# Kernel optimization log

Hardware: AMD Instinct MI355X
Metric: run time of the kernel (lower is better)

The kernel has to match this reference:

```python
import jax, jax.numpy as jnp
import numpy as np
from functools import partial

TAU = 2.0          # leak
VTH = 1.0          # threshold_value
DECAY = 1.0 - 1.0 / TAU  # decay_input=False, v_reset=0: v = v*(1-1/tau) + x
PAD = 3
STRIDE = 1


def heaviside(x):
    # forward of spikingjelly surrogate.ATan (surrogate only changes backward)
    return (x >= 0).astype(x.dtype)


def lif(v, inp):
    """One LIF step: charge, fire, hard reset (v_reset=0)."""
    v = v * DECAY + inp
    s = heaviside(v - VTH)
    v = v * (1.0 - s)
    return v, s


def setup_inputs() -> dict:
    key = jax.random.key(0)
    k1, k2, k3, k4 = jax.random.split(key, 4)
    B, L = 64, 2048
    C, H, NC, K = 128, 256, 10, 7
    x = jax.random.normal(k1, (B, L), dtype=jnp.float32)
    conv_w = jax.random.normal(k2, (C, 1, K), dtype=jnp.float32) * (1.0 / np.sqrt(K))
    W1 = jax.random.normal(k3, (H, C), dtype=jnp.float32) * (1.0 / np.sqrt(C))
    W2 = jax.random.normal(k4, (NC, H), dtype=jnp.float32) * (1.0 / np.sqrt(H))
    return {"x": x, "conv_w": conv_w, "W1": W1, "W2": W2}


def _forward(x, conv_w, W1, W2):
    B = x.shape[0]
    C, H, NC = conv_w.shape[0], W1.shape[0], W2.shape[0]
    # Conv1d(1 -> C): [B, 1, L] -> [B, C, T]
    xc = jax.lax.conv_general_dilated(
        x[:, None, :], conv_w, window_strides=(STRIDE,),
        padding=[(PAD, PAD)], dimension_numbers=("NCH", "OIH", "NCH"))
    T = xc.shape[2]
    xt = jnp.transpose(xc, (2, 0, 1))  # [T, B, C]

    def step(carry, x_t):
        v1, v2, v3, acc = carry
        v1, s1 = lif(v1, x_t)                       # conv LIF  [B, C]
        v2, s2 = lif(v2, s1 @ W1.T)                 # hidden LIF [B, H]
        v3, s3 = lif(v3, s2 @ W2.T)                 # output LIF [B, NC]
        return (v1, v2, v3, acc + s3), None

    zeros = lambda d: jnp.zeros((B, d), dtype=x.dtype)
    init = (zeros(C), zeros(H), zeros(NC), zeros(NC))
    (_, _, _, acc), _ = jax.lax.scan(step, init, xt)
    return acc / T


def reference(x, conv_w, W1, W2):
    return _forward(x, conv_w, W1, W2)
```

## Files before the change

### kernel.cpp

```cpp
#include <hip/hip_runtime.h>
#include <stdint.h>

#define T_STEPS 2048
#define BB 64
#define CC 128
#define HH 256
#define NCLS 10

#define S1_OFF  0
#define DP_OFF  16777216
#define DP2_OFF 16908288
#define S2B_OFF 16924672

typedef int v4i __attribute__((ext_vector_type(4)));

__global__ __launch_bounds__(128) void k0_digits(
    const float* __restrict__ W1, const float* __restrict__ W2,
    signed char* __restrict__ dp, signed char* __restrict__ dp2) {
  const int blk = blockIdx.x;
  const int c = threadIdx.x;
  if (blk < HH) {
    float w = W1[blk * CC + c];
    int q = __float2int_rn(w * 2147483648.0f);
#pragma unroll
    for (int d = 0; d < 3; ++d) {
      int dig = (int)(signed char)(q & 0xff);
      dp[d * (HH * CC) + blk * CC + c] = (signed char)dig;
      q = (q - dig) >> 8;
    }
    dp[3 * (HH * CC) + blk * CC + c] = (signed char)q;
  } else {
    const int nc = blk - HH;
#pragma unroll
    for (int half = 0; half < 2; ++half) {
      int cc = half * 128 + c;
      float w = (nc < NCLS) ? W2[nc * HH + cc] : 0.0f;
      int q = __float2int_rn(w * 2147483648.0f);
#pragma unroll
      for (int d = 0; d < 3; ++d) {
        int dig = (int)(signed char)(q & 0xff);
        dp2[d * (16 * HH) + nc * HH + cc] = (signed char)dig;
        q = (q - dig) >> 8;
      }
      dp2[3 * (16 * HH) + nc * HH + cc] = (signed char)q;
    }
  }
}

__global__ __launch_bounds__(128) void k1_conv_lif1(
    const float* __restrict__ x, const float* __restrict__ cw,
    unsigned char* __restrict__ s1) {
  const int c = threadIdx.x;
  const int b = blockIdx.y;
  const int t0 = blockIdx.x * 128;
  const int ts = t0 - 64;

  float w[7];
#pragma unroll
  for (int k = 0; k < 7; ++k) w[k] = cw[c * 7 + k];

  const float* xb = x + b * 2048;
  float xw[7];
#pragma unroll
  for (int k = 0; k < 7; ++k) {
    int l = ts + k - 3;
    xw[k] = (l >= 0 && l < 2048) ? xb[l] : 0.0f;
  }

  float v = 0.0f;
#pragma unroll 7
  for (int t = ts; t < t0 + 128; ++t) {
    float u = fmaf(w[0], xw[0],
              fmaf(w[1], xw[1],
              fmaf(w[2], xw[2],
              fmaf(w[3], xw[3],
              fmaf(w[4], xw[4],
              fmaf(w[5], xw[5], w[6] * xw[6]))))));
    v = fmaf(v, 0.5f, u);
    bool sp = (v >= 1.0f);
    if (t >= t0) s1[((size_t)t * BB + b) * CC + c] = (unsigned char)(sp ? 1 : 0);
    if (sp) v = 0.0f;
#pragma unroll
    for (int k = 0; k < 6; ++k) xw[k] = xw[k + 1];
    int ln = t + 4;
    xw[6] = (ln >= 0 && ln < 2048) ? xb[ln] : 0.0f;
  }
}

__global__ __launch_bounds__(256, 4) void k2_mfma_lif2(
    const unsigned char* __restrict__ s1, const signed char* __restrict__ dp,
    unsigned char* __restrict__ s2b) {
  const int tid  = threadIdx.x;
  const int lane = tid & 63;
  const int wv   = tid >> 6;
  const int hg   = blockIdx.x;
  const int b    = blockIdx.y;
  const int chunk= blockIdx.z;
  const int t0   = chunk * 256;
  const int nwarm= (chunk == 0) ? 0 : 4;
  const int ts   = t0 - nwarm * 16;
  const int l15  = lane & 15;
  const int lg   = lane >> 4;

  v4i Bf[2][4][2];
#pragma unroll
  for (int n = 0; n < 2; ++n) {
    const int h = hg * 128 + wv * 32 + n * 16 + l15;
#pragma unroll
    for (int d = 0; d < 4; ++d)
#pragma unroll
      for (int kc = 0; kc < 2; ++kc)
        Bf[n][d][kc] = *(const v4i*)(dp + d * (HH * CC) + h * CC + kc * 64 + lg * 16);
  }

  const unsigned char* ap =
      s1 + ((size_t)(ts + l15) * BB + b) * CC + lg * 16;
  v4i Af0 = *(const v4i*)(ap);
  v4i Af1 = *(const v4i*)(ap + 64);
  ap += 16 * BB * CC;

  float v0 = 0.0f, v1 = 0.0f;

  const int nsub = nwarm + 16;
  for (int s = 0; s < nsub; ++s) {
    const int tb = ts + s * 16;

    v4i Pf0 = *(const v4i*)(ap);
    v4i Pf1 = *(const v4i*)(ap + 64);
    ap += 16 * BB * CC;

    float u0[4], u1[4];
#pragma unroll
    for (int n = 0; n < 2; ++n) {
      v4i a0 = {0, 0, 0, 0}, a1 = {0, 0, 0, 0}, a2 = {0, 0, 0, 0}, a3 = {0, 0, 0, 0};
      a0 = __builtin_amdgcn_mfma_i32_16x16x64_i8(Af0, Bf[n][0][0], a0, 0, 0, 0);
      a1 = __builtin_amdgcn_mfma_i32_16x16x64_i8(Af0, Bf[n][1][0], a1, 0, 0, 0);
      a2 = __builtin_amdgcn_mfma_i32_16x16x64_i8(Af0, Bf[n][2][0], a2, 0, 0, 0);
      a3 = __builtin_amdgcn_mfma_i32_16x16x64_i8(Af0, Bf[n][3][0], a3, 0, 0, 0);
      a0 = __builtin_amdgcn_mfma_i32_16x16x64_i8(Af1, Bf[n][0][1], a0, 0, 0, 0);
      a1 = __builtin_amdgcn_mfma_i32_16x16x64_i8(Af1, Bf[n][1][1], a1, 0, 0, 0);
      a2 = __builtin_amdgcn_mfma_i32_16x16x64_i8(Af1, Bf[n][2][1], a2, 0, 0, 0);
      a3 = __builtin_amdgcn_mfma_i32_16x16x64_i8(Af1, Bf[n][3][1], a3, 0, 0, 0);
#pragma unroll
      for (int r = 0; r < 4; ++r) {
        int hi = a3[r] * 256 + a2[r];
        int lo = a1[r] * 256 + a0[r];
        float u = fmaf((float)hi, 0x1p-15f, (float)lo * 0x1p-31f);
        if (n == 0) u0[r] = u; else u1[r] = u;
      }
    }

    unsigned sp0 = 0, sp1 = 0;
#pragma unroll
    for (int g = 0; g < 4; ++g) {
      if (lg == g) {
#pragma unroll
        for (int r = 0; r < 4; ++r) {
          v0 = fmaf(v0, 0.5f, u0[r]); bool a = (v0 >= 1.0f); if (a) v0 = 0.0f;
          sp0 |= (a ? 1u : 0u) << r;
          v1 = fmaf(v1, 0.5f, u1[r]); bool c = (v1 >= 1.0f); if (c) v1 = 0.0f;
          sp1 |= (c ? 1u : 0u) << r;
        }
      }
      if (g < 3) {
        float w0 = __shfl(v0, (lane - 16) & 63);
        float w1 = __shfl(v1, (lane - 16) & 63);
        if (lg == g + 1) { v0 = w0; v1 = w1; }
      }
    }
    v0 = __shfl(v0, 48 + l15);
    v1 = __shfl(v1, 48 + l15);

    if (s >= nwarm) {
      size_t base = ((size_t)(tb + lg * 4) * BB + b) * 256 + hg * 128 + wv * 32 + l15;
#pragma unroll
      for (int r = 0; r < 4; ++r) {
        s2b[base + (size_t)r * (BB * 256)]      = (unsigned char)((sp0 >> r) & 1u);
        s2b[base + (size_t)r * (BB * 256) + 16] = (unsigned char)((sp1 >> r) & 1u);
      }
    }

    Af0 = Pf0; Af1 = Pf1;
  }
}

__global__ __launch_bounds__(64, 4) void k34_gemm3_lif3(
    const unsigned char* __restrict__ s2b, const signed char* __restrict__ dp2,
    float* __restrict__ out) {
  const int lane = threadIdx.x;
  const int l15  = lane & 15;
  const int lg   = lane >> 4;
  const int b    = blockIdx.x;
  const int chunk= blockIdx.y;
  const int t0   = chunk * 128;
  const int nwarm= (chunk == 0) ? 0 : 4;
  const int ts   = t0 - nwarm * 16;

  v4i Bf[4][4];
#pragma unroll
  for (int d = 0; d < 4; ++d)
#pragma unroll
    for (int kc = 0; kc < 4; ++kc)
      Bf[d][kc] = *(const v4i*)(dp2 + d * (16 * HH) + l15 * HH + kc * 64 + lg * 16);

  const unsigned char* ap =
      s2b + ((size_t)(ts + l15) * BB + b) * 256 + lg * 16;
  v4i Af[4];
#pragma unroll
  for (int kc = 0; kc < 4; ++kc) Af[kc] = *(const v4i*)(ap + kc * 64);
  ap += 16 * BB * 256;

  float v = 0.0f, cnt = 0.0f;
  const int nsub = nwarm + 8;
  for (int s = 0; s < nsub; ++s) {
    v4i Pf[4];
#pragma unroll
    for (int kc = 0; kc < 4; ++kc) Pf[kc] = *(const v4i*)(ap + kc * 64);
    ap += 16 * BB * 256;

    v4i a0 = {0, 0, 0, 0}, a1 = {0, 0, 0, 0}, a2 = {0, 0, 0, 0}, a3 = {0, 0, 0, 0};
#pragma unroll
    for (int kc = 0; kc < 4; ++kc) {
      a0 = __builtin_amdgcn_mfma_i32_16x16x64_i8(Af[kc], Bf[0][kc], a0, 0, 0, 0);
      a1 = __builtin_amdgcn_mfma_i32_16x16x64_i8(Af[kc], Bf[1][kc], a1, 0, 0, 0);
      a2 = __builtin_amdgcn_mfma_i32_16x16x64_i8(Af[kc], Bf[2][kc], a2, 0, 0, 0);
      a3 = __builtin_amdgcn_mfma_i32_16x16x64_i8(Af[kc], Bf[3][kc], a3, 0, 0, 0);
    }

    float u[4];
#pragma unroll
    for (int r = 0; r < 4; ++r) {
      int hi = a3[r] * 256 + a2[r];
      int lo = a1[r] * 256 + a0[r];
      u[r] = fmaf((float)hi, 0x1p-15f, (float)lo * 0x1p-31f);
    }

    bool commit = (s >= nwarm);
#pragma unroll
    for (int g = 0; g < 4; ++g) {
      if (lg == g) {
#pragma unroll
        for (int r = 0; r < 4; ++r) {
          v = fmaf(v, 0.5f, u[r]); bool a = (v >= 1.0f); if (a) v = 0.0f;
          if (a && commit) cnt += 1.0f;
        }
      }
      if (g < 3) {
        float w = __shfl(v, (lane - 16) & 63);
        if (lg == g + 1) v = w;
      }
    }
    v = __shfl(v, 48 + l15);

#pragma unroll
    for (int kc = 0; kc < 4; ++kc) Af[kc] = Pf[kc];
  }

  cnt += __shfl_xor(cnt, 16);
  cnt += __shfl_xor(cnt, 32);
  if (lane < NCLS)
    atomicAdd(&out[b * NCLS + lane], cnt * (1.0f / 2048.0f));
}

extern "C" void kernel_launch(void* const* d_in, const int* in_sizes, int n_in,
                              void* d_out, int out_size, void* d_ws, size_t ws_size,
                              hipStream_t stream) {
  const float* x  = (const float*)d_in[0];
  const float* cw = (const float*)d_in[1];
  const float* W1 = (const float*)d_in[2];
  const float* W2 = (const float*)d_in[3];
  float* out = (float*)d_out;

  char* ws = (char*)d_ws;
  unsigned char* s1  = (unsigned char*)(ws + S1_OFF);
  signed char*   dp  = (signed char*)(ws + DP_OFF);
  signed char*   dp2 = (signed char*)(ws + DP2_OFF);
  unsigned char* s2b = (unsigned char*)(ws + S2B_OFF);

  hipMemsetAsync(d_out, 0, 64 * NCLS * sizeof(float), stream);

  k0_digits<<<dim3(HH + 16), 128, 0, stream>>>(W1, W2, dp, dp2);
  k1_conv_lif1<<<dim3(16, 64), 128, 0, stream>>>(x, cw, s1);
  k2_mfma_lif2<<<dim3(2, 64, 8), 256, 0, stream>>>(s1, dp, s2b);
  k34_gemm3_lif3<<<dim3(64, 16), 64, 0, stream>>>(s2b, dp2, out);
  (void)in_sizes; (void)n_in; (void)out_size; (void)ws_size;
}
```

Measured before the change: 149.6 us.

## Merge prep kernels, halve per-wave LIF columns, use bpermute transpose for scan

Merges the digit-split, conv+LIF1 and output-zeroing work into one launch, dropping the memset and a kernel launch. The hidden-layer kernel now gives each wave 16 hidden units instead of 32 and doubles the grid. The serial 4-group shuffle chain for the LIF recurrence is replaced by ds_bpermute gathers, so every lane runs all 16 timesteps for its own column without waiting on other groups. The output kernel uses shorter time chunks with a doubled grid. This adds redundant LIF work per lane and more warm-up overhead relative to useful steps.

```diff
diff --git a/kernel.cpp b/kernel.cpp
--- a/kernel.cpp
+++ b/kernel.cpp
@@ -14,26 +14,67 @@
 
 typedef int v4i __attribute__((ext_vector_type(4)));
 
-__global__ __launch_bounds__(128) void k0_digits(
+__global__ __launch_bounds__(128) void k01_prep(
+    const float* __restrict__ x, const float* __restrict__ cw,
     const float* __restrict__ W1, const float* __restrict__ W2,
-    signed char* __restrict__ dp, signed char* __restrict__ dp2) {
-  const int blk = blockIdx.x;
-  const int c = threadIdx.x;
-  if (blk < HH) {
-    float w = W1[blk * CC + c];
+    unsigned char* __restrict__ s1, signed char* __restrict__ dp,
+    signed char* __restrict__ dp2, float* __restrict__ out) {
+  const int bx = blockIdx.x;
+  const int tidx = threadIdx.x;
+
+  if (bx < 1024) {
+    const int c = tidx;
+    const int b = bx & 63;
+    const int t0 = (bx >> 6) * 128;
+    const int ts = t0 - 64;
+
+    float w[7];
+#pragma unroll
+    for (int k = 0; k < 7; ++k) w[k] = cw[c * 7 + k];
+
+    const float* xb = x + b * 2048;
+    float xw[7];
+#pragma unroll
+    for (int k = 0; k < 7; ++k) {
+      int l = ts + k - 3;
+      xw[k] = (l >= 0 && l < 2048) ? xb[l] : 0.0f;
+    }
+
+    float v = 0.0f;
+#pragma unroll 7
+    for (int t = ts; t < t0 + 128; ++t) {
+      float u = fmaf(w[0], xw[0],
+                fmaf(w[1], xw[1],
+                fmaf(w[2], xw[2],
+                fmaf(w[3], xw[3],
+                fmaf(w[4], xw[4],
+                fmaf(w[5], xw[5], w[6] * xw[6]))))));
+      v = fmaf(v, 0.5f, u);
+      bool sp = (v >= 1.0f);
+      if (t >= t0) s1[((size_t)t * BB + b) * CC + c] = (unsigned char)(sp ? 1 : 0);
+      if (sp) v = 0.0f;
+#pragma unroll
+      for (int k = 0; k < 6; ++k) xw[k] = xw[k + 1];
+      int ln = t + 4;
+      xw[6] = (ln >= 0 && ln < 2048) ? xb[ln] : 0.0f;
+    }
+  } else if (bx < 1280) {
+    const int h = bx - 1024;
+    const int c = tidx;
+    float w = W1[h * CC + c];
     int q = __float2int_rn(w * 2147483648.0f);
 #pragma unroll
     for (int d = 0; d < 3; ++d) {
       int dig = (int)(signed char)(q & 0xff);
-      dp[d * (HH * CC) + blk * CC + c] = (signed char)dig;
+      dp[d * (HH * CC) + h * CC + c] = (signed char)dig;
       q = (q - dig) >> 8;
     }
-    dp[3 * (HH * CC) + blk * CC + c] = (signed char)q;
-  } else {
-    const int nc = blk - HH;
+    dp[3 * (HH * CC) + h * CC + c] = (signed char)q;
+  } else if (bx < 1296) {
+    const int nc = bx - 1280;
 #pragma unroll
     for (int half = 0; half < 2; ++half) {
-      int cc = half * 128 + c;
+      int cc = half * 128 + tidx;
       float w = (nc < NCLS) ? W2[nc * HH + cc] : 0.0f;
       int q = __float2int_rn(w * 2147483648.0f);
 #pragma unroll
@@ -44,46 +85,9 @@
       }
       dp2[3 * (16 * HH) + nc * HH + cc] = (signed char)q;
     }
-  }
-}
-
-__global__ __launch_bounds__(128) void k1_conv_lif1(
-    const float* __restrict__ x, const float* __restrict__ cw,
-    unsigned char* __restrict__ s1) {
-  const int c = threadIdx.x;
-  const int b = blockIdx.y;
-  const int t0 = blockIdx.x * 128;
-  const int ts = t0 - 64;
-
-  float w[7];
-#pragma unroll
-  for (int k = 0; k < 7; ++k) w[k] = cw[c * 7 + k];
-
-  const float* xb = x + b * 2048;
-  float xw[7];
-#pragma unroll
-  for (int k = 0; k < 7; ++k) {
-    int l = ts + k - 3;
-    xw[k] = (l >= 0 && l < 2048) ? xb[l] : 0.0f;
-  }
-
-  float v = 0.0f;
-#pragma unroll 7
-  for (int t = ts; t < t0 + 128; ++t) {
-    float u = fmaf(w[0], xw[0],
-              fmaf(w[1], xw[1],
-              fmaf(w[2], xw[2],
-              fmaf(w[3], xw[3],
-              fmaf(w[4], xw[4],
-              fmaf(w[5], xw[5], w[6] * xw[6]))))));
-    v = fmaf(v, 0.5f, u);
-    bool sp = (v >= 1.0f);
-    if (t >= t0) s1[((size_t)t * BB + b) * CC + c] = (unsigned char)(sp ? 1 : 0);
-    if (sp) v = 0.0f;
-#pragma unroll
-    for (int k = 0; k < 6; ++k) xw[k] = xw[k + 1];
-    int ln = t + 4;
-    xw[6] = (ln >= 0 && ln < 2048) ? xb[ln] : 0.0f;
+  } else {
+#pragma unroll
+    for (int i = 0; i < 5; ++i) out[tidx + 128 * i] = 0.0f;
   }
 }
 
@@ -101,17 +105,14 @@
   const int ts   = t0 - nwarm * 16;
   const int l15  = lane & 15;
   const int lg   = lane >> 4;
-
-  v4i Bf[2][4][2];
-#pragma unroll
-  for (int n = 0; n < 2; ++n) {
-    const int h = hg * 128 + wv * 32 + n * 16 + l15;
-#pragma unroll
-    for (int d = 0; d < 4; ++d)
-#pragma unroll
-      for (int kc = 0; kc < 2; ++kc)
-        Bf[n][d][kc] = *(const v4i*)(dp + d * (HH * CC) + h * CC + kc * 64 + lg * 16);
-  }
+  const int h    = hg * 64 + wv * 16 + l15;
+
+  v4i Bf[4][2];
+#pragma unroll
+  for (int d = 0; d < 4; ++d)
+#pragma unroll
+    for (int kc = 0; kc < 2; ++kc)
+      Bf[d][kc] = *(const v4i*)(dp + d * (HH * CC) + h * CC + kc * 64 + lg * 16);
 
   const unsigned char* ap =
       s1 + ((size_t)(ts + l15) * BB + b) * CC + lg * 16;
@@ -119,7 +120,8 @@
   v4i Af1 = *(const v4i*)(ap + 64);
   ap += 16 * BB * CC;
 
-  float v0 = 0.0f, v1 = 0.0f;
+  const int a4 = l15 * 4;
+  float v = 0.0f;
 
   const int nsub = nwarm + 16;
   for (int s = 0; s < nsub; ++s) {
@@ -129,62 +131,58 @@
     v4i Pf1 = *(const v4i*)(ap + 64);
     ap += 16 * BB * CC;
 
-    float u0[4], u1[4];
-#pragma unroll
-    for (int n = 0; n < 2; ++n) {
-      v4i a0 = {0, 0, 0, 0}, a1 = {0, 0, 0, 0}, a2 = {0, 0, 0, 0}, a3 = {0, 0, 0, 0};
-      a0 = __builtin_amdgcn_mfma_i32_16x16x64_i8(Af0, Bf[n][0][0], a0, 0, 0, 0);
-      a1 = __builtin_amdgcn_mfma_i32_16x16x64_i8(Af0, Bf[n][1][0], a1, 0, 0, 0);
-      a2 = __builtin_amdgcn_mfma_i32_16x16x64_i8(Af0, Bf[n][2][0], a2, 0, 0, 0);
-      a3 = __builtin_amdgcn_mfma_i32_16x16x64_i8(Af0, Bf[n][3][0], a3, 0, 0, 0);
-      a0 = __builtin_amdgcn_mfma_i32_16x16x64_i8(Af1, Bf[n][0][1], a0, 0, 0, 0);
-      a1 = __builtin_amdgcn_mfma_i32_16x16x64_i8(Af1, Bf[n][1][1], a1, 0, 0, 0);
-      a2 = __builtin_amdgcn_mfma_i32_16x16x64_i8(Af1, Bf[n][2][1], a2, 0, 0, 0);
-      a3 = __builtin_amdgcn_mfma_i32_16x16x64_i8(Af1, Bf[n][3][1], a3, 0, 0, 0);
+    v4i a0 = {0, 0, 0, 0}, a1 = {0, 0, 0, 0}, a2 = {0, 0, 0, 0}, a3 = {0, 0, 0, 0};
+    a0 = __builtin_amdgcn_mfma_i32_16x16x64_i8(Af0, Bf[0][0], a0, 0, 0, 0);
+    a1 = __builtin_amdgcn_mfma_i32_16x16x64_i8(Af0, Bf[1][0], a1, 0, 0, 0);
+    a2 = __builtin_amdgcn_mfma_i32_16x16x64_i8(Af0, Bf[2][0], a2, 0, 0, 0);
+    a3 = __builtin_amdgcn_mfma_i32_16x16x64_i8(Af0, Bf[3][0], a3, 0, 0, 0);
+    a0 = __builtin_amdgcn_mfma_i32_16x16x64_i8(Af1, Bf[0][1], a0, 0, 0, 0);
+    a1 = __builtin_amdgcn_mfma_i32_16x16x64_i8(Af1, Bf[1][1], a1, 0, 0, 0);
+    a2 = __builtin_amdgcn_mfma_i32_16x16x64_i8(Af1, Bf[2][1], a2, 0, 0, 0);
+    a3 = __builtin_amdgcn_mfma_i32_16x16x64_i8(Af1, Bf[3][1], a3, 0, 0, 0);
+
+    float u[4];
+#pragma unroll
+    for (int r = 0; r < 4; ++r) {
+      int hi = a3[r] * 256 + a2[r];
+      int lo = a1[r] * 256 + a0[r];
+      u[r] = fmaf((float)hi, 0x1p-15f, (float)lo * 0x1p-31f);
+    }
+
+    float ua[4][4];
+#pragma unroll
+    for (int q = 0; q < 4; ++q) {
+      const int addr = a4 + q * 64;
+#pragma unroll
+      for (int r = 0; r < 4; ++r)
+        ua[q][r] = __int_as_float(
+            __builtin_amdgcn_ds_bpermute(addr, __float_as_int(u[r])));
+    }
+
+    unsigned spbits = 0;
+#pragma unroll
+    for (int q = 0; q < 4; ++q)
 #pragma unroll
       for (int r = 0; r < 4; ++r) {
-        int hi = a3[r] * 256 + a2[r];
-        int lo = a1[r] * 256 + a0[r];
-        float u = fmaf((float)hi, 0x1p-15f, (float)lo * 0x1p-31f);
-        if (n == 0) u0[r] = u; else u1[r] = u;
+        v = fmaf(v, 0.5f, ua[q][r]);
+        bool sp = (v >= 1.0f);
+        if (sp) v = 0.0f;
+        spbits |= (sp ? 1u : 0u) << (q * 4 + r);
       }
-    }
-
-    unsigned sp0 = 0, sp1 = 0;
-#pragma unroll
-    for (int g = 0; g < 4; ++g) {
-      if (lg == g) {
-#pragma unroll
-        for (int r = 0; r < 4; ++r) {
-          v0 = fmaf(v0, 0.5f, u0[r]); bool a = (v0 >= 1.0f); if (a) v0 = 0.0f;
-          sp0 |= (a ? 1u : 0u) << r;
-          v1 = fmaf(v1, 0.5f, u1[r]); bool c = (v1 >= 1.0f); if (c) v1 = 0.0f;
-          sp1 |= (c ? 1u : 0u) << r;
-        }
-      }
-      if (g < 3) {
-        float w0 = __shfl(v0, (lane - 16) & 63);
-        float w1 = __shfl(v1, (lane - 16) & 63);
-        if (lg == g + 1) { v0 = w0; v1 = w1; }
-      }
-    }
-    v0 = __shfl(v0, 48 + l15);
-    v1 = __shfl(v1, 48 + l15);
 
     if (s >= nwarm) {
-      size_t base = ((size_t)(tb + lg * 4) * BB + b) * 256 + hg * 128 + wv * 32 + l15;
-#pragma unroll
-      for (int r = 0; r < 4; ++r) {
-        s2b[base + (size_t)r * (BB * 256)]      = (unsigned char)((sp0 >> r) & 1u);
-        s2b[base + (size_t)r * (BB * 256) + 16] = (unsigned char)((sp1 >> r) & 1u);
-      }
+      size_t base = ((size_t)(tb + lg * 4) * BB + b) * 256 + h;
+#pragma unroll
+      for (int r = 0; r < 4; ++r)
+        s2b[base + (size_t)r * (BB * 256)] =
+            (unsigned char)((spbits >> (lg * 4 + r)) & 1u);
     }
 
     Af0 = Pf0; Af1 = Pf1;
   }
 }
 
-__global__ __launch_bounds__(64, 4) void k34_gemm3_lif3(
+__global__ __launch_bounds__(64) void k34_gemm3_lif3(
     const unsigned char* __restrict__ s2b, const signed char* __restrict__ dp2,
     float* __restrict__ out) {
   const int lane = threadIdx.x;
@@ -192,7 +190,7 @@
   const int lg   = lane >> 4;
   const int b    = blockIdx.x;
   const int chunk= blockIdx.y;
-  const int t0   = chunk * 128;
+  const int t0   = chunk * 64;
   const int nwarm= (chunk == 0) ? 0 : 4;
   const int ts   = t0 - nwarm * 16;
 
@@ -210,8 +208,9 @@
   for (int kc = 0; kc < 4; ++kc) Af[kc] = *(const v4i*)(ap + kc * 64);
   ap += 16 * BB * 256;
 
+  const int a4 = l15 * 4;
   float v = 0.0f, cnt = 0.0f;
-  const int nsub = nwarm + 8;
+  const int nsub = nwarm + 4;
   for (int s = 0; s < nsub; ++s) {
     v4i Pf[4];
 #pragma unroll
@@ -235,29 +234,30 @@
       u[r] = fmaf((float)hi, 0x1p-15f, (float)lo * 0x1p-31f);
     }
 
-    bool commit = (s >= nwarm);
-#pragma unroll
-    for (int g = 0; g < 4; ++g) {
-      if (lg == g) {
-#pragma unroll
-        for (int r = 0; r < 4; ++r) {
-          v = fmaf(v, 0.5f, u[r]); bool a = (v >= 1.0f); if (a) v = 0.0f;
-          if (a && commit) cnt += 1.0f;
-        }
+    float ua[4][4];
+#pragma unroll
+    for (int q = 0; q < 4; ++q) {
+      const int addr = a4 + q * 64;
+#pragma unroll
+      for (int r = 0; r < 4; ++r)
+        ua[q][r] = __int_as_float(
+            __builtin_amdgcn_ds_bpermute(addr, __float_as_int(u[r])));
+    }
+
+    float inc = (s >= nwarm) ? 1.0f : 0.0f;
+#pragma unroll
+    for (int q = 0; q < 4; ++q)
+#pragma unroll
+      for (int r = 0; r < 4; ++r) {
+        v = fmaf(v, 0.5f, ua[q][r]);
+        bool sp = (v >= 1.0f);
+        if (sp) { v = 0.0f; cnt += inc; }
       }
-      if (g < 3) {
-        float w = __shfl(v, (lane - 16) & 63);
-        if (lg == g + 1) v = w;
-      }
-    }
-    v = __shfl(v, 48 + l15);
 
 #pragma unroll
     for (int kc = 0; kc < 4; ++kc) Af[kc] = Pf[kc];
   }
 
-  cnt += __shfl_xor(cnt, 16);
-  cnt += __shfl_xor(cnt, 32);
   if (lane < NCLS)
     atomicAdd(&out[b * NCLS + lane], cnt * (1.0f / 2048.0f));
 }
@@ -277,11 +277,8 @@
   signed char*   dp2 = (signed char*)(ws + DP2_OFF);
   unsigned char* s2b = (unsigned char*)(ws + S2B_OFF);
 
-  hipMemsetAsync(d_out, 0, 64 * NCLS * sizeof(float), stream);
-
-  k0_digits<<<dim3(HH + 16), 128, 0, stream>>>(W1, W2, dp, dp2);
-  k1_conv_lif1<<<dim3(16, 64), 128, 0, stream>>>(x, cw, s1);
-  k2_mfma_lif2<<<dim3(2, 64, 8), 256, 0, stream>>>(s1, dp, s2b);
-  k34_gemm3_lif3<<<dim3(64, 16), 64, 0, stream>>>(s2b, dp2, out);
+  k01_prep<<<dim3(1297), 128, 0, stream>>>(x, cw, W1, W2, s1, dp, dp2, out);
+  k2_mfma_lif2<<<dim3(4, 64, 8), 256, 0, stream>>>(s1, dp, s2b);
+  k34_gemm3_lif3<<<dim3(64, 32), 64, 0, stream>>>(s2b, dp2, out);
   (void)in_sizes; (void)n_in; (void)out_size; (void)ws_size;
 }
```

Result: slower. 158.1 us (+5.7%).
